# Kernel optimization log

Measured on AMD Instinct MI355X. Metric: run time of the kernel, lower is better.

## Reference

```python
import jax, jax.numpy as jnp
import numpy as np

N, E, R, D = 50000, 1600000, 512, 64

def _mlp(x, w1, b1, w2, b2):
    # torch nn.Linear: y = x @ W.T + b ; Sequential(Linear(2D,D), ReLU, Linear(D,D))
    h = jax.nn.relu(x @ w1.T + b1)
    return h @ w2.T + b2

def setup_inputs() -> dict:
    key = jax.random.key(0)
    ks = jax.random.split(key, 8)
    edge_index = jax.random.randint(ks[0], (2, E), 0, N, dtype=jnp.int64)
    edge_type = jax.random.randint(ks[1], (E,), 0, R, dtype=jnp.int64)
    rel = jax.random.normal(ks[2], (R, D), dtype=jnp.float32)
    s2d = 1.0 / np.sqrt(2.0 * D)
    sd = 1.0 / np.sqrt(1.0 * D)
    w1a = jax.random.normal(ks[3], (D, 2 * D), dtype=jnp.float32) * s2d
    w2a = jax.random.normal(ks[4], (D, D), dtype=jnp.float32) * sd
    w1b = jax.random.normal(ks[5], (D, 2 * D), dtype=jnp.float32) * s2d
    w2b = jax.random.normal(ks[6], (D, D), dtype=jnp.float32) * sd
    zeros = jnp.zeros((D,), jnp.float32)
    strength = jnp.full((1,), 0.1, dtype=jnp.float32)
    return {
        'edge_index': edge_index, 'edge_type': edge_type,
        'relation_embeddings': rel,
        'w1a': w1a, 'b1a': zeros, 'w2a': w2a, 'b2a': zeros,
        'w1b': w1b, 'b1b': zeros, 'w2b': w2b, 'b2b': zeros,
        'strength': strength, 'num_nodes': N,
    }

def reference(edge_index, edge_type, relation_embeddings,
              w1a, b1a, w2a, b2a, w1b, b1b, w2b, b2b,
              strength, num_nodes):
    # Batched version of compute_entity_relation_features over all entities.
    # For entity e: feat = mean of relation embeddings over edges incident to e
    # (each edge counted once, as in the boolean-mask original).
    src, dst = edge_index[0], edge_index[1]
    rel_e = relation_embeddings[edge_type]                      # [E, D]
    not_self = (src != dst).astype(rel_e.dtype)                 # avoid double-count self-loops
    sum_feat = (jax.ops.segment_sum(rel_e, src, num_segments=num_nodes)
                + jax.ops.segment_sum(rel_e * not_self[:, None], dst, num_segments=num_nodes))
    ones = jnp.ones((rel_e.shape[0],), rel_e.dtype)
    deg = (jax.ops.segment_sum(ones, src, num_segments=num_nodes)
           + jax.ops.segment_sum(not_self, dst, num_segments=num_nodes))  # [N]
    has_edge = deg > 0
    rel_ctx = relation_embeddings.mean(axis=0)                  # [D]
    feat = jnp.where(has_edge[:, None], sum_feat / jnp.maximum(deg, 1.0)[:, None], rel_ctx)

    # interaction branch: cat(feat, global relation context) -> MLP a
    ctx_b = jnp.broadcast_to(rel_ctx, feat.shape)
    interaction = _mlp(jnp.concatenate([feat, ctx_b], axis=-1), w1a, b1a, w2a, b2a)
    # context branch: neighbor_context == entity_relation_avg == feat
    ctx_feat_n = _mlp(jnp.concatenate([feat, feat], axis=-1), w1b, b1b, w2b, b2b)
    # has_neighbor: at least one non-self-loop incident edge
    nbr_deg = (jax.ops.segment_sum(not_self, src, num_segments=num_nodes)
               + jax.ops.segment_sum(not_self, dst, num_segments=num_nodes))
    has_nbr = nbr_deg > 0
    context_feat = jnp.where(has_nbr[:, None], ctx_feat_n, interaction)

    s = jnp.clip(strength[0], 0.0, 0.3)
    enhanced = (1.0 - s) * feat + s * context_feat
    # entities with no incident edges fall back to mean relation embedding
    return jnp.where(has_edge[:, None], enhanced, rel_ctx)
```

## Files before the change

kernel.cpp:

```cpp
#include <hip/hip_runtime.h>

#define DD   64
#define WSH  6
#define WSZ  64
#define TILE 4096
#define ALGN 16
#define GMAX 1024
#define SMAX 1024
#define CAP  8192
#define LSTG 20480
#define RK   512
#define RTP  520
#define NWB  256

typedef unsigned int u32;
typedef unsigned short u16;
typedef __attribute__((ext_vector_type(4))) float f32x4;
typedef __attribute__((ext_vector_type(4))) u32 u32x4;
typedef __attribute__((ext_vector_type(8))) short short8;


__device__ inline u32 f2bf(float x) {
    u32 u = __float_as_uint(x);
    return (u + 0x7FFFu + ((u >> 16) & 1u)) >> 16;
}
__device__ inline float bf2f(u32 b) { return __uint_as_float(b << 16); }
__device__ inline int swz16(int row, int col) {
    return row * 64 + ((((col >> 3) ^ (row & 7)) << 3) | (col & 7));
}
__device__ inline u32 pack_bf_hi(float lo, float hi) {
    return __builtin_amdgcn_perm(__float_as_uint(hi), __float_as_uint(lo),
                                 0x07060302u);
}

__global__ __launch_bounds__(512)
void k_prep(const float* __restrict__ rel, int R, float* __restrict__ ctxpart,
            u16* __restrict__ relT, const float* __restrict__ w1,
            const float* __restrict__ w2, u16* __restrict__ w1t,
            u16* __restrict__ w2t, int* __restrict__ gcur, int G) {
    if (blockIdx.x == 8) {
        for (int i = threadIdx.x; i < DD * DD; i += 512) {
            int j = i >> 6, k = i & 63;
            w1t[i] = (u16)f2bf(w1[j * 2 * DD + k] + w1[j * 2 * DD + DD + k]);
            w2t[i] = (u16)f2bf(w2[i]);
        }
        for (int i = threadIdx.x; i < G + 1; i += 512) gcur[i] = 0;
        return;
    }
    __shared__ float part[8][DD];
    int k0 = blockIdx.x * (RK / 8);
    int d  = threadIdx.x & 63;
    int rg = threadIdx.x >> 6;
    float s = 0.f;
    #pragma unroll
    for (int i = 0; i < 8; ++i) {
        int k = k0 + rg * 8 + i;
        float v = rel[k * DD + d];
        relT[d * RK + k] = (u16)f2bf(v);
        s += v;
    }
    part[rg][d] = s;
    __syncthreads();
    if (threadIdx.x < DD) {
        float t = 0.f;
        #pragma unroll
        for (int i = 0; i < 8; ++i) t += part[i][threadIdx.x];
        ctxpart[blockIdx.x * DD + threadIdx.x] = t;
    }
}

__global__ __launch_bounds__(512)
void k_gplace(const int* __restrict__ src, const int* __restrict__ dst,
              const int* __restrict__ etype, int* __restrict__ gcur,
              u16* __restrict__ es, u32* __restrict__ selflist,
              int* __restrict__ slcnt, int E, int G) {
    __shared__ int lcnt[GMAX];
    __shared__ int lbase[GMAX];
    __shared__ int loff[GMAX];
    __shared__ int lcur[GMAX];
    __shared__ __align__(32) u16 stage[LSTG];
    int tid = threadIdx.x;
    for (int i = tid; i < GMAX; i += 512) lcnt[i] = 0;
    __syncthreads();
    int t0 = blockIdx.x * TILE;
    int t1 = min(t0 + TILE, E);
    for (int i = t0 + tid; i < t1; i += 512) {
        int s = src[i], d = dst[i];
        atomicAdd(&lcnt[s >> WSH], 1);
        if (s != d) atomicAdd(&lcnt[d >> WSH], 1);
    }
    __syncthreads();
    for (int i = tid; i < GMAX; i += 512)
        loff[i] = (i < G) ? ((lcnt[i] + ALGN - 1) & ~(ALGN - 1)) : 0;
    __syncthreads();
    for (int d2 = 1; d2 < GMAX; d2 <<= 1) {
        int v0 = (tid >= d2) ? loff[tid - d2] : 0;
        int v1 = loff[tid + 512 - d2];
        __syncthreads();
        loff[tid] += v0;
        loff[tid + 512] += v1;
        __syncthreads();
    }
    for (int g = tid; g < G; g += 512) {
        int c = lcnt[g];
        int pad = (c + ALGN - 1) & ~(ALGN - 1);
        int st = loff[g] - pad;
        loff[g] = st;
        lcur[g] = st;
        lbase[g] = c ? atomicAdd(&gcur[g], pad) : 0;
    }
    __syncthreads();
    for (int i = t0 + tid; i < t1; i += 512) {
        int s = src[i], d = dst[i];
        u32 t = (u32)etype[i];
        int gs = s >> WSH;
        int p = atomicAdd(&lcur[gs], 1);
        stage[p] = (u16)((u32)(s & 63) | (t << 6));
        if (s != d) {
            int gd = d >> WSH;
            int q = atomicAdd(&lcur[gd], 1);
            stage[q] = (u16)((u32)(d & 63) | (t << 6));
        } else {
            int p2 = atomicAdd(slcnt, 1);
            if (p2 < SMAX) selflist[p2] = ((u32)s << 9) | t;
        }
    }
    __syncthreads();
    for (int g = tid; g < G; g += 512) {
        int c = lcnt[g];
        if (!c) continue;
        int pad = (c + ALGN - 1) & ~(ALGN - 1);
        int st = loff[g];
        for (int p = st + c; p < st + pad; ++p) stage[p] = 0xFFFFu;
    }
    __syncthreads();
    for (int g = tid; g < G; g += 512) {
        int c = lcnt[g];
        if (!c) continue;
        int pad = (c + ALGN - 1) & ~(ALGN - 1);
        int st = loff[g];
        int gb = lbase[g];
        u16* dp = es + (size_t)g * CAP + gb;
        for (int off = 0; off < pad; off += 16) {
            if (gb + off + 16 <= CAP) {
                u32x4 a = *(const u32x4*)(stage + st + off);
                u32x4 b = *(const u32x4*)(stage + st + off + 8);
                *(u32x4*)(dp + off) = a;
                *(u32x4*)(dp + off + 8) = b;
            }
        }
    }
}

__global__ __launch_bounds__(1024, 1)
void k_win(const u16* __restrict__ es, const int* __restrict__ gcur,
           const u16* __restrict__ relT, const u16* __restrict__ w1t,
           const u16* __restrict__ w2t, const float* __restrict__ ctxpart,
           int R, const float* __restrict__ b1, const float* __restrict__ b2,
           const float* __restrict__ strength, float* __restrict__ out,
           const u32* __restrict__ selflist, const int* __restrict__ slcnt,
           const float* __restrict__ w1a, const float* __restrict__ b1a,
           const float* __restrict__ w2a, const float* __restrict__ b2a,
           int N, int GW) {
    __shared__ __align__(16) u32 Hn[WSZ * RK / 8];
    __shared__ __align__(16) u16 rt[WSZ * RTP];
    __shared__ __align__(16) u16 w1s[DD * DD];
    __shared__ __align__(16) u16 w2s[DD * DD];
    __shared__ __align__(16) u16 Fb[DD * DD];
    __shared__ __align__(16) u16 H1b[DD * DD];
    __shared__ int cnts[WSZ];
    __shared__ int selfc[WSZ];
    __shared__ float invd[WSZ];
    __shared__ float b1s[DD], b2s[DD], ctx_s[DD];

    int tid = threadIdx.x;
    int lane = tid & 63;
    int wv = tid >> 6;
    if (tid < DD) {
        b1s[tid] = b1[tid]; b2s[tid] = b2[tid];
        float t = 0.f;
        #pragma unroll
        for (int i = 0; i < 8; ++i) t += ctxpart[i * DD + tid];
        ctx_s[tid] = t / (float)R;
    }
    for (int i = tid; i < 4096; i += 1024) {
        int col = i >> 6, k8 = i & 63;
        *(short8*)(rt + col * RTP + k8 * 8) =
            *(const short8*)(relT + col * RK + k8 * 8);
    }
    if (tid < 512) {
        int col = tid >> 3, kk = (tid & 7) * 8;
        *(short8*)(w1s + swz16(col, kk)) = *(const short8*)(w1t + col * DD + kk);
        *(short8*)(w2s + swz16(col, kk)) = *(const short8*)(w2t + col * DD + kk);
    }
    float sc = fminf(fmaxf(strength[0], 0.f), 0.3f);
    int scount = min(*slcnt, SMAX);

    int mb = wv >> 2, nbq = wv & 3;
    int arow = mb * 16 + (lane & 15);
    int kgrp = (lane >> 4) * 8;
    int kg = kgrp >> 3;
    int col = nbq * 16 + (lane & 15);

    int w = blockIdx.x;
    u32x4 myv = {0u, 0u, 0u, 0u};
    bool have = false;
    if (w < GW) {
        int cntE = min(gcur[w], CAP);
        int nv = cntE >> 3;
        if (tid < nv) { myv = ((const u32x4*)(es + (size_t)w * CAP))[tid]; have = true; }
    }

    for (; w < GW; ) {
        int wn = w + gridDim.x;
        __syncthreads();
        for (int i = tid; i < 4096; i += 1024) Hn[i] = 0;
        if (tid < WSZ) selfc[tid] = 0;
        __syncthreads();
        if (have) {
            #pragma unroll
            for (int c = 0; c < 4; ++c) {
                u32 v2 = myv[c];
                #pragma unroll
                for (int h = 0; h < 2; ++h) {
                    u32 v = h ? (v2 >> 16) : (v2 & 0xFFFFu);
                    if (v == 0xFFFFu) continue;
                    int r = (int)(v & 63);
                    int t = (int)((v >> 6) & 0x1FF);
                    int word = r * 64 + ((t >> 3) ^ ((r & 7) << 2));
                    atomicAdd(&Hn[word], 1u << ((t & 7) * 4));
                }
            }
        }
        for (int i = tid; i < scount; i += 1024) {
            int n = (int)(selflist[i] >> 9);
            if ((n >> WSH) == w) atomicAdd(&selfc[n & 63], 1);
        }
        u32x4 nxtv = {0u, 0u, 0u, 0u};
        bool haven = false;
        if (wn < GW) {
            int cn = min(gcur[wn], CAP) >> 3;
            if (tid < cn) { nxtv = ((const u32x4*)(es + (size_t)wn * CAP))[tid]; haven = true; }
        }
        __syncthreads();
        if (tid < 512) {
            int row = tid >> 3;
            int s = 0;
            int w0 = row * 64 + (tid & 7) * 8;
            #pragma unroll
            for (int i = 0; i < 8; ++i) {
                u32 v = Hn[w0 + i];
                u32 a = (v & 0x0F0F0F0Fu) + ((v >> 4) & 0x0F0F0F0Fu);
                s += (int)((a & 0xFF) + ((a >> 8) & 0xFF) +
                           ((a >> 16) & 0xFF) + (a >> 24));
            }
            s += __shfl_down(s, 4); s += __shfl_down(s, 2); s += __shfl_down(s, 1);
            if ((tid & 7) == 0) { cnts[row] = s; invd[row] = s ? 1.f / s : 0.f; }
        }
        __syncthreads();

        u32 aw[16];
        {
            int abase = arow * 64;
            #pragma unroll
            for (int ks = 0; ks < 16; ++ks)
                aw[ks] = Hn[abase + ((ks * 4 + kg) ^ ((arow & 7) << 2))];
        }
        f32x4 acc = {0.f, 0.f, 0.f, 0.f};
        #pragma unroll
        for (int q = 0; q < 16; ++q) {
            int k8 = (q * 32 + kgrp) >> 3;
            u32 v = aw[q];
            u32 af32[4];
            #pragma unroll
            for (int e = 0; e < 4; ++e) {
                float g0 = (float)((v >> (8 * e)) & 0xFu);
                float g1 = (float)((v >> (8 * e + 4)) & 0xFu);
                af32[e] = pack_bf_hi(g0, g1);
            }
            short8 af = *(short8*)af32;
            const short8* bp = (const short8*)(rt + col * RTP + k8 * 8);
            acc = __builtin_amdgcn_mfma_f32_16x16x32_bf16(af, *bp, acc, 0, 0, 0);
        }
        #pragma unroll
        for (int r = 0; r < 4; ++r) {
            int row = mb * 16 + (lane >> 4) * 4 + r;
            Fb[swz16(row, col)] = (u16)f2bf(acc[r] * invd[row]);
        }
        __syncthreads();

        f32x4 a2 = {0.f, 0.f, 0.f, 0.f};
        #pragma unroll
        for (int ks = 0; ks < 2; ++ks) {
            int kb = ks * 32 + kgrp;
            const short8* ap = (const short8*)
                (Fb + arow * 64 + (((kb >> 3) ^ (arow & 7)) << 3));
            const short8* bp = (const short8*)
                (w1s + col * 64 + (((kb >> 3) ^ (col & 7)) << 3));
            a2 = __builtin_amdgcn_mfma_f32_16x16x32_bf16(*ap, *bp, a2, 0, 0, 0);
        }
        #pragma unroll
        for (int r = 0; r < 4; ++r) {
            int row = mb * 16 + (lane >> 4) * 4 + r;
            H1b[swz16(row, col)] = (u16)f2bf(fmaxf(a2[r] + b1s[col], 0.f));
        }
        __syncthreads();

        f32x4 a3 = {0.f, 0.f, 0.f, 0.f};
        #pragma unroll
        for (int ks = 0; ks < 2; ++ks) {
            int kb = ks * 32 + kgrp;
            const short8* ap = (const short8*)
                (H1b + arow * 64 + (((kb >> 3) ^ (arow & 7)) << 3));
            const short8* bp = (const short8*)
                (w2s + col * 64 + (((kb >> 3) ^ (col & 7)) << 3));
            a3 = __builtin_amdgcn_mfma_f32_16x16x32_bf16(*ap, *bp, a3, 0, 0, 0);
        }
        #pragma unroll
        for (int r = 0; r < 4; ++r) {
            int row = mb * 16 + (lane >> 4) * 4 + r;
            int n = (w << WSH) + row;
            if (n >= N) continue;
            int c = cnts[row];
            if (c > 0 && selfc[row] == c) continue;
            float o = a3[r] + b2s[col];
            float f = bf2f(Fb[swz16(row, col)]);
            out[n * DD + col] = (c == 0) ? ctx_s[col] : (1.f - sc) * f + sc * o;
        }
        if (wv == 0) {
            int c = cnts[lane];
            bool fl = (c > 0) && (selfc[lane] == c) && ((w << WSH) + lane < N);
            unsigned long long m = __ballot(fl);
            float cx = ctx_s[lane];
            while (m) {
                int rr = __ffsll(m) - 1;
                m &= m - 1;
                int n = (w << WSH) + rr;
                float f = bf2f(Fb[swz16(rr, lane)]);
                float h = b1a[lane];
                for (int k = 0; k < DD; ++k)
                    h = fmaf(__shfl(f, k), w1a[lane * 2 * DD + k], h);
                for (int k = 0; k < DD; ++k)
                    h = fmaf(__shfl(cx, k), w1a[lane * 2 * DD + DD + k], h);
                h = fmaxf(h, 0.f);
                float o = b2a[lane];
                for (int k = 0; k < DD; ++k)
                    o = fmaf(__shfl(h, k), w2a[lane * DD + k], o);
                out[n * DD + lane] = (1.f - sc) * f + sc * o;
            }
        }
        myv = nxtv; have = haven; w = wn;
    }
}

extern "C" void kernel_launch(void* const* d_in, const int* in_sizes, int n_in,
                              void* d_out, int out_size, void* d_ws, size_t ws_size,
                              hipStream_t stream) {
    const int*   edge_index = (const int*)d_in[0];
    const int*   etype      = (const int*)d_in[1];
    const float* rel        = (const float*)d_in[2];
    const float* w1a        = (const float*)d_in[3];
    const float* b1a        = (const float*)d_in[4];
    const float* w2a        = (const float*)d_in[5];
    const float* b2a        = (const float*)d_in[6];
    const float* w1b        = (const float*)d_in[7];
    const float* b1b        = (const float*)d_in[8];
    const float* w2b        = (const float*)d_in[9];
    const float* b2b        = (const float*)d_in[10];
    const float* strength   = (const float*)d_in[11];

    int E = in_sizes[0] / 2;
    int R = in_sizes[2] / DD;
    int N = out_size / DD;
    int GW = (N + WSZ - 1) >> WSH;

    float* out = (float*)d_out;
    char*  p   = (char*)d_ws;

    int*   gcur    = (int*)p;   p += (size_t)GW * sizeof(int);
    int*   slcnt   = (int*)p;   p += sizeof(int);
    float* ctxpart = (float*)p; p += 8 * DD * sizeof(float);
    p = (char*)(((size_t)p + 15) & ~(size_t)15);
    u16*   relT     = (u16*)p; p += (size_t)RK * DD * sizeof(u16);
    u16*   w1t      = (u16*)p; p += (size_t)DD * DD * sizeof(u16);
    u16*   w2t      = (u16*)p; p += (size_t)DD * DD * sizeof(u16);
    u32*   selflist = (u32*)p; p += (size_t)SMAX * sizeof(u32);
    u16*   es       = (u16*)p;

    k_prep<<<9, 512, 0, stream>>>(rel, R, ctxpart, relT, w1b, w2b, w1t, w2t,
                                  gcur, GW);

    const int* src = edge_index;
    const int* dst = edge_index + E;
    int nb = (E + TILE - 1) / TILE;

    k_gplace<<<nb, 512, 0, stream>>>(src, dst, etype, gcur, es,
                                     selflist, slcnt, E, GW);

    k_win<<<NWB, 1024, 0, stream>>>(es, gcur, relT, w1t, w2t, ctxpart, R,
                                    b1b, b2b, strength, out,
                                    selflist, slcnt, w1a, b1a, w2a, b2a,
                                    N, GW);
}
```

Baseline: 60.55 us.

## Process two node windows per block iteration with dual-column MFMA tiles

```diff
diff --git a/kernel.cpp b/kernel.cpp
--- a/kernel.cpp
+++ b/kernel.cpp
@@ -19,6 +19,9 @@
 typedef __attribute__((ext_vector_type(4))) u32 u32x4;
 typedef __attribute__((ext_vector_type(8))) short short8;
 
+
+#define BAR() do { asm volatile("s_waitcnt lgkmcnt(0)" ::: "memory"); \
+                   __builtin_amdgcn_s_barrier(); } while (0)
 
 __device__ inline u32 f2bf(float x) {
     u32 u = __float_as_uint(x);
@@ -152,6 +155,23 @@
     }
 }
 
+__device__ inline void scatter_hn(u32x4 v4, bool have, u32* Hw) {
+    if (!have) return;
+    #pragma unroll
+    for (int c = 0; c < 4; ++c) {
+        u32 v2 = v4[c];
+        #pragma unroll
+        for (int h = 0; h < 2; ++h) {
+            u32 v = h ? (v2 >> 16) : (v2 & 0xFFFFu);
+            if (v == 0xFFFFu) continue;
+            int r = (int)(v & 63);
+            int t = (int)((v >> 6) & 0x1FF);
+            int word = r * 64 + ((t >> 3) ^ ((r & 7) << 2));
+            atomicAdd(&Hw[word], 1u << ((t & 7) * 4));
+        }
+    }
+}
+
 __global__ __launch_bounds__(1024, 1)
 void k_win(const u16* __restrict__ es, const int* __restrict__ gcur,
            const u16* __restrict__ relT, const u16* __restrict__ w1t,
@@ -162,15 +182,14 @@
            const float* __restrict__ w1a, const float* __restrict__ b1a,
            const float* __restrict__ w2a, const float* __restrict__ b2a,
            int N, int GW) {
-    __shared__ __align__(16) u32 Hn[WSZ * RK / 8];
+    __shared__ __align__(16) u32 Hn[2][WSZ * RK / 8];
     __shared__ __align__(16) u16 rt[WSZ * RTP];
     __shared__ __align__(16) u16 w1s[DD * DD];
     __shared__ __align__(16) u16 w2s[DD * DD];
-    __shared__ __align__(16) u16 Fb[DD * DD];
-    __shared__ __align__(16) u16 H1b[DD * DD];
-    __shared__ int cnts[WSZ];
-    __shared__ int selfc[WSZ];
-    __shared__ float invd[WSZ];
+    __shared__ __align__(16) u16 Fb[2][DD * DD];
+    __shared__ int cnts[2][WSZ];
+    __shared__ int selfc[2][WSZ];
+    __shared__ float invd[2][WSZ];
     __shared__ float b1s[DD], b2s[DD], ctx_s[DD];
 
     int tid = threadIdx.x;
@@ -184,92 +203,101 @@
         ctx_s[tid] = t / (float)R;
     }
     for (int i = tid; i < 4096; i += 1024) {
-        int col = i >> 6, k8 = i & 63;
-        *(short8*)(rt + col * RTP + k8 * 8) =
-            *(const short8*)(relT + col * RK + k8 * 8);
+        int c = i >> 6, k8 = i & 63;
+        *(short8*)(rt + c * RTP + k8 * 8) =
+            *(const short8*)(relT + c * RK + k8 * 8);
     }
     if (tid < 512) {
-        int col = tid >> 3, kk = (tid & 7) * 8;
-        *(short8*)(w1s + swz16(col, kk)) = *(const short8*)(w1t + col * DD + kk);
-        *(short8*)(w2s + swz16(col, kk)) = *(const short8*)(w2t + col * DD + kk);
+        int c = tid >> 3, kk = (tid & 7) * 8;
+        *(short8*)(w1s + swz16(c, kk)) = *(const short8*)(w1t + c * DD + kk);
+        *(short8*)(w2s + swz16(c, kk)) = *(const short8*)(w2t + c * DD + kk);
     }
     float sc = fminf(fmaxf(strength[0], 0.f), 0.3f);
     int scount = min(*slcnt, SMAX);
 
-    int mb = wv >> 2, nbq = wv & 3;
+    int ww  = wv & 1;
+    int wq  = wv >> 1;
+    int mb  = wq & 3;
+    int nb0 = wq >> 2;
     int arow = mb * 16 + (lane & 15);
     int kgrp = (lane >> 4) * 8;
     int kg = kgrp >> 3;
-    int col = nbq * 16 + (lane & 15);
-
-    int w = blockIdx.x;
-    u32x4 myv = {0u, 0u, 0u, 0u};
-    bool have = false;
-    if (w < GW) {
-        int cntE = min(gcur[w], CAP);
-        int nv = cntE >> 3;
-        if (tid < nv) { myv = ((const u32x4*)(es + (size_t)w * CAP))[tid]; have = true; }
-    }
-
-    for (; w < GW; ) {
-        int wn = w + gridDim.x;
-        __syncthreads();
-        for (int i = tid; i < 4096; i += 1024) Hn[i] = 0;
-        if (tid < WSZ) selfc[tid] = 0;
-        __syncthreads();
-        if (have) {
-            #pragma unroll
-            for (int c = 0; c < 4; ++c) {
-                u32 v2 = myv[c];
-                #pragma unroll
-                for (int h = 0; h < 2; ++h) {
-                    u32 v = h ? (v2 >> 16) : (v2 & 0xFFFFu);
-                    if (v == 0xFFFFu) continue;
-                    int r = (int)(v & 63);
-                    int t = (int)((v >> 6) & 0x1FF);
-                    int word = r * 64 + ((t >> 3) ^ ((r & 7) << 2));
-                    atomicAdd(&Hn[word], 1u << ((t & 7) * 4));
-                }
-            }
-        }
+    int col0 = nb0 * 16 + (lane & 15);
+    int col1 = col0 + 32;
+
+    int npair = (GW + 1) >> 1;
+    int wp = blockIdx.x;
+    u32x4 va = {0u,0u,0u,0u}, vb = {0u,0u,0u,0u};
+    bool ha = false, hb = false;
+    if (wp < npair) {
+        int wA = 2 * wp, wB = wA + 1;
+        int nvA = min(gcur[wA], CAP) >> 3;
+        if (tid < nvA) { va = ((const u32x4*)(es + (size_t)wA * CAP))[tid]; ha = true; }
+        if (wB < GW) {
+            int nvB = min(gcur[wB], CAP) >> 3;
+            if (tid < nvB) { vb = ((const u32x4*)(es + (size_t)wB * CAP))[tid]; hb = true; }
+        }
+    }
+
+    for (; wp < npair; ) {
+        int wA = 2 * wp, wB = wA + 1;
+        int wpn = wp + gridDim.x;
+        BAR();
+        {
+            u32x4 z = {0u,0u,0u,0u};
+            u32x4* hz = (u32x4*)Hn;
+            hz[tid] = z; hz[tid + 1024] = z;
+        }
+        if (tid < 2 * WSZ) selfc[tid >> 6][tid & 63] = 0;
+        u32x4 na = {0u,0u,0u,0u}, nb = {0u,0u,0u,0u};
+        bool hna = false, hnb = false;
+        if (wpn < npair) {
+            int wAn = 2 * wpn, wBn = wAn + 1;
+            int nvA = min(gcur[wAn], CAP) >> 3;
+            if (tid < nvA) { na = ((const u32x4*)(es + (size_t)wAn * CAP))[tid]; hna = true; }
+            if (wBn < GW) {
+                int nvB = min(gcur[wBn], CAP) >> 3;
+                if (tid < nvB) { nb = ((const u32x4*)(es + (size_t)wBn * CAP))[tid]; hnb = true; }
+            }
+        }
+        BAR();
+        scatter_hn(va, ha, Hn[0]);
+        scatter_hn(vb, hb, Hn[1]);
         for (int i = tid; i < scount; i += 1024) {
             int n = (int)(selflist[i] >> 9);
-            if ((n >> WSH) == w) atomicAdd(&selfc[n & 63], 1);
-        }
-        u32x4 nxtv = {0u, 0u, 0u, 0u};
-        bool haven = false;
-        if (wn < GW) {
-            int cn = min(gcur[wn], CAP) >> 3;
-            if (tid < cn) { nxtv = ((const u32x4*)(es + (size_t)wn * CAP))[tid]; haven = true; }
-        }
-        __syncthreads();
-        if (tid < 512) {
-            int row = tid >> 3;
+            int wd = n >> WSH;
+            if (wd == wA) atomicAdd(&selfc[0][n & 63], 1);
+            else if (wd == wB) atomicAdd(&selfc[1][n & 63], 1);
+        }
+        BAR();
+        {
+            int w2 = tid >> 9;
+            int row = (tid >> 3) & 63;
             int s = 0;
             int w0 = row * 64 + (tid & 7) * 8;
             #pragma unroll
             for (int i = 0; i < 8; ++i) {
-                u32 v = Hn[w0 + i];
+                u32 v = Hn[w2][w0 + i];
                 u32 a = (v & 0x0F0F0F0Fu) + ((v >> 4) & 0x0F0F0F0Fu);
                 s += (int)((a & 0xFF) + ((a >> 8) & 0xFF) +
                            ((a >> 16) & 0xFF) + (a >> 24));
             }
             s += __shfl_down(s, 4); s += __shfl_down(s, 2); s += __shfl_down(s, 1);
-            if ((tid & 7) == 0) { cnts[row] = s; invd[row] = s ? 1.f / s : 0.f; }
-        }
-        __syncthreads();
+            if ((tid & 7) == 0) { cnts[w2][row] = s; invd[w2][row] = s ? 1.f / s : 0.f; }
+        }
+        BAR();
 
         u32 aw[16];
         {
             int abase = arow * 64;
             #pragma unroll
             for (int ks = 0; ks < 16; ++ks)
-                aw[ks] = Hn[abase + ((ks * 4 + kg) ^ ((arow & 7) << 2))];
-        }
-        f32x4 acc = {0.f, 0.f, 0.f, 0.f};
+                aw[ks] = Hn[ww][abase + ((ks * 4 + kg) ^ ((arow & 7) << 2))];
+        }
+        f32x4 acc0 = {0.f,0.f,0.f,0.f}, acc1 = {0.f,0.f,0.f,0.f};
         #pragma unroll
         for (int q = 0; q < 16; ++q) {
-            int k8 = (q * 32 + kgrp) >> 3;
+            int k8 = q * 4 + kg;
             u32 v = aw[q];
             u32 af32[4];
             #pragma unroll
@@ -279,64 +307,85 @@
                 af32[e] = pack_bf_hi(g0, g1);
             }
             short8 af = *(short8*)af32;
-            const short8* bp = (const short8*)(rt + col * RTP + k8 * 8);
-            acc = __builtin_amdgcn_mfma_f32_16x16x32_bf16(af, *bp, acc, 0, 0, 0);
+            acc0 = __builtin_amdgcn_mfma_f32_16x16x32_bf16(
+                af, *(const short8*)(rt + col0 * RTP + k8 * 8), acc0, 0, 0, 0);
+            acc1 = __builtin_amdgcn_mfma_f32_16x16x32_bf16(
+                af, *(const short8*)(rt + col1 * RTP + k8 * 8), acc1, 0, 0, 0);
         }
         #pragma unroll
         for (int r = 0; r < 4; ++r) {
             int row = mb * 16 + (lane >> 4) * 4 + r;
-            Fb[swz16(row, col)] = (u16)f2bf(acc[r] * invd[row]);
-        }
-        __syncthreads();
-
-        f32x4 a2 = {0.f, 0.f, 0.f, 0.f};
+            float iv = invd[ww][row];
+            Fb[ww][swz16(row, col0)] = (u16)f2bf(acc0[r] * iv);
+            Fb[ww][swz16(row, col1)] = (u16)f2bf(acc1[r] * iv);
+        }
+        BAR();
+
+        u16* H1 = (u16*)Hn[ww];
+        f32x4 a20 = {0.f,0.f,0.f,0.f}, a21 = {0.f,0.f,0.f,0.f};
         #pragma unroll
         for (int ks = 0; ks < 2; ++ks) {
             int kb = ks * 32 + kgrp;
             const short8* ap = (const short8*)
-                (Fb + arow * 64 + (((kb >> 3) ^ (arow & 7)) << 3));
-            const short8* bp = (const short8*)
-                (w1s + col * 64 + (((kb >> 3) ^ (col & 7)) << 3));
-            a2 = __builtin_amdgcn_mfma_f32_16x16x32_bf16(*ap, *bp, a2, 0, 0, 0);
-        }
+                (Fb[ww] + arow * 64 + (((kb >> 3) ^ (arow & 7)) << 3));
+            a20 = __builtin_amdgcn_mfma_f32_16x16x32_bf16(*ap,
+                *(const short8*)(w1s + col0 * 64 + (((kb >> 3) ^ (col0 & 7)) << 3)),
+                a20, 0, 0, 0);
+            a21 = __builtin_amdgcn_mfma_f32_16x16x32_bf16(*ap,
+                *(const short8*)(w1s + col1 * 64 + (((kb >> 3) ^ (col1 & 7)) << 3)),
+                a21, 0, 0, 0);
+        }
+        BAR();
         #pragma unroll
         for (int r = 0; r < 4; ++r) {
             int row = mb * 16 + (lane >> 4) * 4 + r;
-            H1b[swz16(row, col)] = (u16)f2bf(fmaxf(a2[r] + b1s[col], 0.f));
-        }
-        __syncthreads();
-
-        f32x4 a3 = {0.f, 0.f, 0.f, 0.f};
+            H1[swz16(row, col0)] = (u16)f2bf(fmaxf(a20[r] + b1s[col0], 0.f));
+            H1[swz16(row, col1)] = (u16)f2bf(fmaxf(a21[r] + b1s[col1], 0.f));
+        }
+        BAR();
+
+        f32x4 a30 = {0.f,0.f,0.f,0.f}, a31 = {0.f,0.f,0.f,0.f};
         #pragma unroll
         for (int ks = 0; ks < 2; ++ks) {
             int kb = ks * 32 + kgrp;
             const short8* ap = (const short8*)
-                (H1b + arow * 64 + (((kb >> 3) ^ (arow & 7)) << 3));
-            const short8* bp = (const short8*)
-                (w2s + col * 64 + (((kb >> 3) ^ (col & 7)) << 3));
-            a3 = __builtin_amdgcn_mfma_f32_16x16x32_bf16(*ap, *bp, a3, 0, 0, 0);
-        }
+                (H1 + arow * 64 + (((kb >> 3) ^ (arow & 7)) << 3));
+            a30 = __builtin_amdgcn_mfma_f32_16x16x32_bf16(*ap,
+                *(const short8*)(w2s + col0 * 64 + (((kb >> 3) ^ (col0 & 7)) << 3)),
+                a30, 0, 0, 0);
+            a31 = __builtin_amdgcn_mfma_f32_16x16x32_bf16(*ap,
+                *(const short8*)(w2s + col1 * 64 + (((kb >> 3) ^ (col1 & 7)) << 3)),
+                a31, 0, 0, 0);
+        }
+        int wcur = ww ? wB : wA;
         #pragma unroll
         for (int r = 0; r < 4; ++r) {
             int row = mb * 16 + (lane >> 4) * 4 + r;
-            int n = (w << WSH) + row;
+            int n = (wcur << WSH) + row;
             if (n >= N) continue;
-            int c = cnts[row];
-            if (c > 0 && selfc[row] == c) continue;
-            float o = a3[r] + b2s[col];
-            float f = bf2f(Fb[swz16(row, col)]);
-            out[n * DD + col] = (c == 0) ? ctx_s[col] : (1.f - sc) * f + sc * o;
-        }
-        if (wv == 0) {
-            int c = cnts[lane];
-            bool fl = (c > 0) && (selfc[lane] == c) && ((w << WSH) + lane < N);
+            int c = cnts[ww][row];
+            if (c > 0 && selfc[ww][row] == c) continue;
+            #pragma unroll
+            for (int q = 0; q < 2; ++q) {
+                int col = q ? col1 : col0;
+                float o = (q ? a31[r] : a30[r]) + b2s[col];
+                float f = bf2f(Fb[ww][swz16(row, col)]);
+                out[n * DD + col] = (c == 0) ? ctx_s[col] : (1.f - sc) * f + sc * o;
+            }
+        }
+        if (wv < 2) {
+            int wsel = wv;
+            int wdw = wsel ? wB : wA;
+            int c = cnts[wsel][lane];
+            bool fl = (c > 0) && (selfc[wsel][lane] == c) &&
+                      ((wdw << WSH) + lane < N) && (wdw < GW);
             unsigned long long m = __ballot(fl);
             float cx = ctx_s[lane];
             while (m) {
                 int rr = __ffsll(m) - 1;
                 m &= m - 1;
-                int n = (w << WSH) + rr;
-                float f = bf2f(Fb[swz16(rr, lane)]);
+                int n = (wdw << WSH) + rr;
+                float f = bf2f(Fb[wsel][swz16(rr, lane)]);
                 float h = b1a[lane];
                 for (int k = 0; k < DD; ++k)
                     h = fmaf(__shfl(f, k), w1a[lane * 2 * DD + k], h);
@@ -349,7 +398,7 @@
                 out[n * DD + lane] = (1.f - sc) * f + sc * o;
             }
         }
-        myv = nxtv; have = haven; w = wn;
+        va = na; vb = nb; ha = hna; hb = hnb; wp = wpn;
     }
 }
 
```

Result: faster. 54.77 us (median of 3 runs) (-9.6%).
